# Kernel optimization log

Hardware: AMD Instinct MI355X
Metric: run time of the kernel (lower is better)

Reference implementation:

```python
import jax, jax.numpy as jnp
import numpy as np

C_IN = 1.0
C_OUT = 1.0
N_NODES = 10000
D_IN = 256
D_OUT = 256
N_EDGES = 320000
MIN_NORM = 1e-15
BALL_EPS = 4e-3  # float32 boundary eps used by HGCN PoincareBall


def _norm(x):
    return jnp.maximum(jnp.linalg.norm(x, axis=-1, keepdims=True), MIN_NORM)


def _artanh(x):
    x = jnp.clip(x, -1.0 + 1e-7, 1.0 - 1e-7)
    return 0.5 * (jnp.log1p(x) - jnp.log1p(-x))


def proj(x, c):
    norm = _norm(x)
    maxnorm = (1.0 - BALL_EPS) / jnp.sqrt(c)
    return jnp.where(norm > maxnorm, x / norm * maxnorm, x)


def expmap0(u, c):
    sc = jnp.sqrt(c)
    un = _norm(u)
    return jnp.tanh(sc * un) * u / (sc * un)


def logmap0(p, c):
    sc = jnp.sqrt(c)
    pn = _norm(p)
    return _artanh(sc * pn) * p / (sc * pn)


def mobius_add(x, y, c):
    x2 = jnp.sum(x * x, -1, keepdims=True)
    y2 = jnp.sum(y * y, -1, keepdims=True)
    xy = jnp.sum(x * y, -1, keepdims=True)
    num = (1 + 2 * c * xy + c * y2) * x + (1 - c * x2) * y
    denom = 1 + 2 * c * xy + c * c * x2 * y2
    return num / jnp.maximum(denom, MIN_NORM)


def mobius_matvec(m, x, c):
    sc = jnp.sqrt(c)
    xn = _norm(x)
    mx = x @ m.T  # [N, D_out]
    mxn = _norm(mx)
    res = jnp.tanh(mxn / xn * _artanh(sc * xn)) * mx / (mxn * sc)
    cond = jnp.all(mx == 0, axis=-1, keepdims=True)
    return jnp.where(cond, jnp.zeros_like(res), res)


def setup_inputs() -> dict:
    key = jax.random.key(0)
    k = jax.random.split(key, 6)
    x = jax.random.normal(k[0], (N_NODES, D_IN), jnp.float32) * 0.05
    x = proj(x, C_IN)  # valid points on the Poincare ball
    weight = jax.random.normal(k[1], (D_OUT, D_IN), jnp.float32) * (1.0 / np.sqrt(D_IN))
    bias = jax.random.normal(k[2], (D_OUT,), jnp.float32) * 0.01
    adj_val = jax.random.uniform(k[3], (N_EDGES,), jnp.float32) * (1.0 / 32.0)
    adj_row = jnp.sort(jax.random.randint(k[4], (N_EDGES,), 0, N_NODES, jnp.int32))
    adj_col = jax.random.randint(k[5], (N_EDGES,), 0, N_NODES, jnp.int32)
    return {"x": x, "weight": weight, "bias": bias, "adj_val": adj_val,
            "adj_row": adj_row, "adj_col": adj_col}


def reference(x, weight, bias, adj_val, adj_row, adj_col):
    # --- HypLinear: mobius matvec + hyperbolic bias ---
    h = proj(mobius_matvec(weight, x, C_IN), C_IN)
    hyp_bias = proj(expmap0(bias[None, :], C_IN), C_IN)  # proj_tan0 is identity
    h = proj(mobius_add(h, hyp_bias, C_IN), C_IN)
    # --- HypAgg: tangent-space sparse aggregation ---
    x_t = logmap0(h, C_IN)  # [N, D_out]
    msgs = adj_val[:, None] * x_t[adj_col]  # [E, D_out]
    support_t = jax.ops.segment_sum(msgs, adj_row, num_segments=N_NODES)
    h = proj(expmap0(support_t, C_IN), C_IN)
    # --- HypAct: act in tangent space, remap with c_out ---
    xt = jax.nn.relu(logmap0(h, C_IN))
    return proj(expmap0(xt, C_OUT), C_OUT)
```

## Files before the change

### kernel.cpp

```cpp
#include <hip/hip_runtime.h>
#include <math.h>

#define D 256
#define MAXNORM (1.0f - 4e-3f)
#define MIN_NORM 1e-15f

typedef _Float16 v8h __attribute__((ext_vector_type(8)));
typedef _Float16 h4  __attribute__((ext_vector_type(4)));
typedef float    v4f __attribute__((ext_vector_type(4)));

__device__ __forceinline__ float wave_reduce_sum(float v) {
    #pragma unroll
    for (int m = 32; m >= 1; m >>= 1) v += __shfl_xor(v, m, 64);
    return v;
}

__device__ __forceinline__ float dot4(const float4& a, const float4& b) {
    return a.x * b.x + a.y * b.y + a.z * b.z + a.w * b.w;
}

__device__ __forceinline__ float artanh_clip(float x) {
    x = fminf(fmaxf(x, -1.0f + 1e-7f), 1.0f - 1e-7f);
    return 0.5f * (log1pf(x) - log1pf(-x));
}

__global__ __launch_bounds__(256) void prep_kernel(
    const float* __restrict__ bias, const float* __restrict__ W,
    const int* __restrict__ rows,
    float* __restrict__ HB, _Float16* __restrict__ Wh,
    int* __restrict__ rowptr, int N, int E)
{
    const int b = blockIdx.x, t = threadIdx.x;
    const int e = b * 256 + t;

    if (e < E) {
        int r1 = rows[e];
        if (e == 0) {
            for (int r = 0; r <= r1; ++r) rowptr[r] = 0;
        } else {
            int r0 = rows[e - 1];
            for (int r = r0 + 1; r <= r1; ++r) rowptr[r] = e;
        }
        if (e == E - 1) {
            for (int r = r1 + 1; r <= N; ++r) rowptr[r] = E;
        }
    }

    if (b < 64) {
        int i = b * 256 + t;
        float4 v = ((const float4*)W)[i];
        h4 o; o[0] = (_Float16)v.x; o[1] = (_Float16)v.y;
        o[2] = (_Float16)v.z; o[3] = (_Float16)v.w;
        *(h4*)(Wh + 4 * (size_t)i) = o;
    }

    if (b == 64 && t < 64) {
        int l = t;
        float4 v = *(const float4*)(bias + 4 * l);
        float bn = fmaxf(sqrtf(wave_reduce_sum(dot4(v, v))), MIN_NORM);
        float f = tanhf(bn) / bn;
        float4 h = make_float4(v.x * f, v.y * f, v.z * f, v.w * f);
        float hn = fmaxf(sqrtf(wave_reduce_sum(dot4(h, h))), MIN_NORM);
        float s = (hn > MAXNORM) ? (MAXNORM / hn) : 1.0f;
        h.x *= s; h.y *= s; h.z *= s; h.w *= s;
        *(float4*)(HB + 4 * l) = h;
        float y2 = wave_reduce_sum(dot4(h, h));
        if (l == 0) HB[D] = y2;
    }
}

#define AS16 264

__global__ __launch_bounds__(256) void gemmrow_kernel(
    const float* __restrict__ X, const _Float16* __restrict__ Wh,
    const float* __restrict__ HB, _Float16* __restrict__ XT, int N)
{
    __shared__ _Float16 As[16 * AS16];
    __shared__ float xnsq[16];
    __shared__ float part_s[16][4];
    __shared__ float part_d[16][4];
    __shared__ float Arow[16], Brow[16];

    const int t = threadIdx.x;
    const int r0 = blockIdx.x * 16;

    {
        const int r = t >> 4, q2 = t & 15;
        const int grow = r0 + r;
        float ss = 0.0f;
        #pragma unroll
        for (int j = 0; j < 4; ++j) {
            const int fi = q2 + j * 16;
            float4 v = make_float4(0.f, 0.f, 0.f, 0.f);
            if (grow < N) v = ((const float4*)X)[(size_t)grow * 64 + fi];
            ss += dot4(v, v);
            h4 hv; hv[0] = (_Float16)v.x; hv[1] = (_Float16)v.y;
            hv[2] = (_Float16)v.z; hv[3] = (_Float16)v.w;
            *(h4*)&As[r * AS16 + fi * 4] = hv;
        }
        ss += __shfl_xor(ss, 1, 64);
        ss += __shfl_xor(ss, 2, 64);
        ss += __shfl_xor(ss, 4, 64);
        ss += __shfl_xor(ss, 8, 64);
        if (q2 == 0) xnsq[r] = ss;
    }
    __syncthreads();

    const int w  = t >> 6;
    const int l  = t & 63;
    const int lm = l & 15;
    const int q  = l >> 4;

    v4f acc[4];
    #pragma unroll
    for (int ct = 0; ct < 4; ++ct)
        #pragma unroll
        for (int i = 0; i < 4; ++i) acc[ct][i] = 0.0f;

    const _Float16* WhB = Wh + (size_t)(64 * w + lm) * 256 + q * 8;

    #pragma unroll
    for (int kc = 0; kc < 8; ++kc) {
        v8h a = *(const v8h*)&As[lm * AS16 + kc * 32 + q * 8];
        #pragma unroll
        for (int ct = 0; ct < 4; ++ct) {
            v8h bfr = *(const v8h*)(WhB + (size_t)ct * 16 * 256 + kc * 32);
            acc[ct] = __builtin_amdgcn_mfma_f32_16x16x32_f16(a, bfr, acc[ct], 0, 0, 0);
        }
    }

    float yv[4];
    #pragma unroll
    for (int ct = 0; ct < 4; ++ct) yv[ct] = HB[64 * w + ct * 16 + lm];

    {
        float s_[4], d_[4];
        #pragma unroll
        for (int i = 0; i < 4; ++i) {
            float s = 0.f, d = 0.f;
            #pragma unroll
            for (int ct = 0; ct < 4; ++ct) {
                float v = acc[ct][i];
                s = fmaf(v, v, s);
                d = fmaf(v, yv[ct], d);
            }
            #pragma unroll
            for (int m = 1; m <= 8; m <<= 1) {
                s += __shfl_xor(s, m, 64);
                d += __shfl_xor(d, m, 64);
            }
            s_[i] = s; d_[i] = d;
        }
        if (lm == 0) {
            #pragma unroll
            for (int i = 0; i < 4; ++i) {
                part_s[q * 4 + i][w] = s_[i];
                part_d[q * 4 + i][w] = d_[i];
            }
        }
    }
    __syncthreads();

    if (t < 16) {
        float mx2 = part_s[t][0] + part_s[t][1] + part_s[t][2] + part_s[t][3];
        float mxy = part_d[t][0] + part_d[t][1] + part_d[t][2] + part_d[t][3];
        float y2  = HB[D];
        float xn  = fmaxf(sqrtf(xnsq[t]), MIN_NORM);
        float mxn = fmaxf(sqrtf(mx2), MIN_NORM);
        float r  = (mxn / xn) * artanh_clip(xn);
        float th = tanhf(r);
        float f  = th / mxn;
        float hn = fmaxf(th, MIN_NORM);
        float s  = (hn > MAXNORM) ? (MAXNORM / hn) : 1.0f;
        float fs = f * s;
        float x2 = th * th * s * s;
        float xy  = fs * mxy;
        float ch  = 1.0f + 2.0f * xy + y2;
        float cy  = 1.0f - x2;
        float inv = 1.0f / fmaxf(1.0f + 2.0f * xy + x2 * y2, MIN_NORM);
        float alpha = ch * fs * inv;
        float beta  = cy * inv;
        float gss = alpha * alpha * mx2 + 2.0f * alpha * beta * mxy + beta * beta * y2;
        float gn  = fmaxf(sqrtf(gss), MIN_NORM);
        float s2  = (gn > MAXNORM) ? (MAXNORM / gn) : 1.0f;
        float pn  = fmaxf(gn * s2, MIN_NORM);
        float lf  = artanh_clip(pn) / pn;
        Arow[t] = lf * s2 * alpha;
        Brow[t] = lf * s2 * beta;
    }
    __syncthreads();

    #pragma unroll
    for (int i = 0; i < 4; ++i) {
        const int rr = q * 4 + i;
        const int row = r0 + rr;
        if (row < N) {
            float A = Arow[rr], B = Brow[rr];
            #pragma unroll
            for (int ct = 0; ct < 4; ++ct) {
                float v = fmaf(A, acc[ct][i], B * yv[ct]);
                XT[(size_t)row * 256 + 64 * w + ct * 16 + lm] = (_Float16)v;
            }
        }
    }
}

__global__ __launch_bounds__(256) void agg_kernel(
    const int* __restrict__ rowptr, const int* __restrict__ cols,
    const float* __restrict__ vals, const _Float16* __restrict__ XT,
    float* __restrict__ OUT, int N)
{
    const int wq = __builtin_amdgcn_readfirstlane(threadIdx.x >> 6);
    const int node = blockIdx.x * 4 + wq;
    const int l = threadIdx.x & 63;
    if (node >= N) return;

    const int start = rowptr[node];
    const int end   = rowptr[node + 1];

    const h4* xt4 = (const h4*)XT;
    float4 acc = make_float4(0.f, 0.f, 0.f, 0.f);

    for (int g = start; g < end; g += 16) {
        int   cbuf[16];
        float vbuf[16];
        #pragma unroll
        for (int u = 0; u < 16; ++u) {
            int ee = g + u;
            bool ok = ee < end;
            int ec = ok ? ee : (end - 1);
            cbuf[u] = cols[ec];
            vbuf[u] = ok ? vals[ec] : 0.0f;
        }
        h4 m[16];
        #pragma unroll
        for (int u = 0; u < 16; ++u)
            m[u] = xt4[(size_t)cbuf[u] * 64 + l];
        #pragma unroll
        for (int u = 0; u < 16; ++u) {
            acc.x = fmaf(vbuf[u], (float)m[u][0], acc.x);
            acc.y = fmaf(vbuf[u], (float)m[u][1], acc.y);
            acc.z = fmaf(vbuf[u], (float)m[u][2], acc.z);
            acc.w = fmaf(vbuf[u], (float)m[u][3], acc.w);
        }
    }

    float un = fmaxf(sqrtf(wave_reduce_sum(dot4(acc, acc))), MIN_NORM);
    float f = tanhf(un) / un;
    float4 h = make_float4(acc.x * f, acc.y * f, acc.z * f, acc.w * f);
    float hn = fmaxf(sqrtf(wave_reduce_sum(dot4(h, h))), MIN_NORM);
    float s = (hn > MAXNORM) ? (MAXNORM / hn) : 1.0f;
    h.x *= s; h.y *= s; h.z *= s; h.w *= s;
    float pn = fmaxf(hn * s, MIN_NORM);
    float lf = artanh_clip(pn) / pn;
    float4 tt = make_float4(fmaxf(h.x * lf, 0.f), fmaxf(h.y * lf, 0.f),
                            fmaxf(h.z * lf, 0.f), fmaxf(h.w * lf, 0.f));
    float un2 = fmaxf(sqrtf(wave_reduce_sum(dot4(tt, tt))), MIN_NORM);
    float f2 = tanhf(un2) / un2;
    float4 o = make_float4(tt.x * f2, tt.y * f2, tt.z * f2, tt.w * f2);
    float on = fmaxf(sqrtf(wave_reduce_sum(dot4(o, o))), MIN_NORM);
    float s2 = (on > MAXNORM) ? (MAXNORM / on) : 1.0f;

    v4f ov;
    ov[0] = o.x * s2; ov[1] = o.y * s2; ov[2] = o.z * s2; ov[3] = o.w * s2;
    __builtin_nontemporal_store(ov, (v4f*)(OUT + (size_t)node * D + 4 * l));
}

extern "C" void kernel_launch(void* const* d_in, const int* in_sizes, int n_in,
                              void* d_out, int out_size, void* d_ws, size_t ws_size,
                              hipStream_t stream) {
    const float* X    = (const float*)d_in[0];
    const float* W    = (const float*)d_in[1];
    const float* bias = (const float*)d_in[2];
    const float* vals = (const float*)d_in[3];
    const int*   rows = (const int*)d_in[4];
    const int*   cols = (const int*)d_in[5];
    float* OUT = (float*)d_out;

    const int N = in_sizes[0] / D;
    const int E = in_sizes[3];

    int*      rowptr = (int*)d_ws;
    float*    HB = (float*)d_ws + 10240;
    _Float16* Wh = (_Float16*)((float*)d_ws + 10240 + 512);
    _Float16* XT = (_Float16*)((float*)d_ws + 10240 + 512 + 32768);

    prep_kernel<<<(E + 255) / 256, 256, 0, stream>>>(bias, W, rows, HB, Wh, rowptr, N, E);
    gemmrow_kernel<<<(N + 15) / 16, 256, 0, stream>>>(X, Wh, HB, XT, N);
    int wave_blocks = (N + 3) / 4;
    agg_kernel<<<wave_blocks, 256, 0, stream>>>(rowptr, cols, vals, XT, OUT, N);
}
```

Baseline: 110.9 us.

## Fuse prep, GEMM and aggregation into one cooperative kernel with grid syncs

```diff
diff --git a/kernel.cpp b/kernel.cpp
--- a/kernel.cpp
+++ b/kernel.cpp
@@ -1,9 +1,13 @@
 #include <hip/hip_runtime.h>
+#include <hip/hip_cooperative_groups.h>
 #include <math.h>
+
+namespace cg = cooperative_groups;
 
 #define D 256
 #define MAXNORM (1.0f - 4e-3f)
 #define MIN_NORM 1e-15f
+#define COOP_GRID 512
 
 typedef _Float16 v8h __attribute__((ext_vector_type(8)));
 typedef _Float16 h4  __attribute__((ext_vector_type(4)));
@@ -22,6 +26,245 @@
 __device__ __forceinline__ float artanh_clip(float x) {
     x = fminf(fmaxf(x, -1.0f + 1e-7f), 1.0f - 1e-7f);
     return 0.5f * (log1pf(x) - log1pf(-x));
+}
+
+#define AS16 264
+
+__global__ __launch_bounds__(256, 2) void fused_coop_kernel(
+    const float* __restrict__ X, const float* __restrict__ W,
+    const float* __restrict__ bias, const float* __restrict__ vals,
+    const int* __restrict__ rows, const int* __restrict__ cols,
+    int* __restrict__ rowptr, _Float16* __restrict__ Wh,
+    float* __restrict__ HB, _Float16* __restrict__ XT,
+    float* __restrict__ OUT, int N, int E)
+{
+    __shared__ _Float16 As[16 * AS16];
+    __shared__ float xnsq[16];
+    __shared__ float part_s[16][4];
+    __shared__ float part_d[16][4];
+    __shared__ float Arow[16], Brow[16];
+
+    const int bid = blockIdx.x;
+    const int t = threadIdx.x;
+
+    for (int e = bid * 256 + t; e < E; e += COOP_GRID * 256) {
+        int r1 = rows[e];
+        if (e == 0) {
+            for (int r = 0; r <= r1; ++r) rowptr[r] = 0;
+        } else {
+            int rp = rows[e - 1];
+            for (int r = rp + 1; r <= r1; ++r) rowptr[r] = e;
+        }
+        if (e == E - 1) {
+            for (int r = r1 + 1; r <= N; ++r) rowptr[r] = E;
+        }
+    }
+    {
+        int i = bid * 256 + t;
+        if (i < 16384) {
+            float4 v = ((const float4*)W)[i];
+            h4 o; o[0] = (_Float16)v.x; o[1] = (_Float16)v.y;
+            o[2] = (_Float16)v.z; o[3] = (_Float16)v.w;
+            *(h4*)(Wh + 4 * (size_t)i) = o;
+        }
+    }
+    if (bid == 0 && t < 64) {
+        int l = t;
+        float4 v = *(const float4*)(bias + 4 * l);
+        float bn = fmaxf(sqrtf(wave_reduce_sum(dot4(v, v))), MIN_NORM);
+        float f = tanhf(bn) / bn;
+        float4 h = make_float4(v.x * f, v.y * f, v.z * f, v.w * f);
+        float hn = fmaxf(sqrtf(wave_reduce_sum(dot4(h, h))), MIN_NORM);
+        float s = (hn > MAXNORM) ? (MAXNORM / hn) : 1.0f;
+        h.x *= s; h.y *= s; h.z *= s; h.w *= s;
+        *(float4*)(HB + 4 * l) = h;
+        float y2 = wave_reduce_sum(dot4(h, h));
+        if (l == 0) HB[D] = y2;
+    }
+
+    cg::this_grid().sync();
+
+    const int NT = (N + 15) / 16;
+    const int w  = t >> 6;
+    const int l  = t & 63;
+    const int lm = l & 15;
+    const int q  = l >> 4;
+
+    for (int tile = bid; tile < NT; tile += COOP_GRID) {
+        const int r0 = tile * 16;
+
+        {
+            const int r = t >> 4, q2 = t & 15;
+            const int grow = r0 + r;
+            float ss = 0.0f;
+            #pragma unroll
+            for (int j = 0; j < 4; ++j) {
+                const int fi = q2 + j * 16;
+                float4 v = make_float4(0.f, 0.f, 0.f, 0.f);
+                if (grow < N) v = ((const float4*)X)[(size_t)grow * 64 + fi];
+                ss += dot4(v, v);
+                h4 hv; hv[0] = (_Float16)v.x; hv[1] = (_Float16)v.y;
+                hv[2] = (_Float16)v.z; hv[3] = (_Float16)v.w;
+                *(h4*)&As[r * AS16 + fi * 4] = hv;
+            }
+            ss += __shfl_xor(ss, 1, 64);
+            ss += __shfl_xor(ss, 2, 64);
+            ss += __shfl_xor(ss, 4, 64);
+            ss += __shfl_xor(ss, 8, 64);
+            if (q2 == 0) xnsq[r] = ss;
+        }
+        __syncthreads();
+
+        v4f acc[4];
+        #pragma unroll
+        for (int ct = 0; ct < 4; ++ct)
+            #pragma unroll
+            for (int i = 0; i < 4; ++i) acc[ct][i] = 0.0f;
+
+        const _Float16* WhB = Wh + (size_t)(64 * w + lm) * 256 + q * 8;
+
+        #pragma unroll
+        for (int kc = 0; kc < 8; ++kc) {
+            v8h a = *(const v8h*)&As[lm * AS16 + kc * 32 + q * 8];
+            #pragma unroll
+            for (int ct = 0; ct < 4; ++ct) {
+                v8h bfr = *(const v8h*)(WhB + (size_t)ct * 16 * 256 + kc * 32);
+                acc[ct] = __builtin_amdgcn_mfma_f32_16x16x32_f16(a, bfr, acc[ct], 0, 0, 0);
+            }
+        }
+
+        float yv[4];
+        #pragma unroll
+        for (int ct = 0; ct < 4; ++ct) yv[ct] = HB[64 * w + ct * 16 + lm];
+
+        {
+            float s_[4], d_[4];
+            #pragma unroll
+            for (int i = 0; i < 4; ++i) {
+                float s = 0.f, d = 0.f;
+                #pragma unroll
+                for (int ct = 0; ct < 4; ++ct) {
+                    float v = acc[ct][i];
+                    s = fmaf(v, v, s);
+                    d = fmaf(v, yv[ct], d);
+                }
+                #pragma unroll
+                for (int m = 1; m <= 8; m <<= 1) {
+                    s += __shfl_xor(s, m, 64);
+                    d += __shfl_xor(d, m, 64);
+                }
+                s_[i] = s; d_[i] = d;
+            }
+            if (lm == 0) {
+                #pragma unroll
+                for (int i = 0; i < 4; ++i) {
+                    part_s[q * 4 + i][w] = s_[i];
+                    part_d[q * 4 + i][w] = d_[i];
+                }
+            }
+        }
+        __syncthreads();
+
+        if (t < 16) {
+            float mx2 = part_s[t][0] + part_s[t][1] + part_s[t][2] + part_s[t][3];
+            float mxy = part_d[t][0] + part_d[t][1] + part_d[t][2] + part_d[t][3];
+            float y2  = HB[D];
+            float xn  = fmaxf(sqrtf(xnsq[t]), MIN_NORM);
+            float mxn = fmaxf(sqrtf(mx2), MIN_NORM);
+            float r  = (mxn / xn) * artanh_clip(xn);
+            float th = tanhf(r);
+            float f  = th / mxn;
+            float hn = fmaxf(th, MIN_NORM);
+            float s  = (hn > MAXNORM) ? (MAXNORM / hn) : 1.0f;
+            float fs = f * s;
+            float x2 = th * th * s * s;
+            float xy  = fs * mxy;
+            float ch  = 1.0f + 2.0f * xy + y2;
+            float cy  = 1.0f - x2;
+            float inv = 1.0f / fmaxf(1.0f + 2.0f * xy + x2 * y2, MIN_NORM);
+            float alpha = ch * fs * inv;
+            float beta  = cy * inv;
+            float gss = alpha * alpha * mx2 + 2.0f * alpha * beta * mxy + beta * beta * y2;
+            float gn  = fmaxf(sqrtf(gss), MIN_NORM);
+            float s2  = (gn > MAXNORM) ? (MAXNORM / gn) : 1.0f;
+            float pn  = fmaxf(gn * s2, MIN_NORM);
+            float lf  = artanh_clip(pn) / pn;
+            Arow[t] = lf * s2 * alpha;
+            Brow[t] = lf * s2 * beta;
+        }
+        __syncthreads();
+
+        #pragma unroll
+        for (int i = 0; i < 4; ++i) {
+            const int rr = q * 4 + i;
+            const int row = r0 + rr;
+            if (row < N) {
+                float A = Arow[rr], B = Brow[rr];
+                #pragma unroll
+                for (int ct = 0; ct < 4; ++ct) {
+                    float v = fmaf(A, acc[ct][i], B * yv[ct]);
+                    XT[(size_t)row * 256 + 64 * w + ct * 16 + lm] = (_Float16)v;
+                }
+            }
+        }
+        __syncthreads();
+    }
+
+    cg::this_grid().sync();
+
+    const int wq = __builtin_amdgcn_readfirstlane(t >> 6);
+    const h4* xt4 = (const h4*)XT;
+
+    for (int node = bid * 4 + wq; node < N; node += COOP_GRID * 4) {
+        const int start = rowptr[node];
+        const int end   = rowptr[node + 1];
+
+        float4 acc2 = make_float4(0.f, 0.f, 0.f, 0.f);
+
+        for (int g = start; g < end; g += 16) {
+            int   cbuf[16];
+            float vbuf[16];
+            #pragma unroll
+            for (int u = 0; u < 16; ++u) {
+                int ee = g + u;
+                bool ok = ee < end;
+                int ec = ok ? ee : (end - 1);
+                cbuf[u] = cols[ec];
+                vbuf[u] = ok ? vals[ec] : 0.0f;
+            }
+            h4 m[16];
+            #pragma unroll
+            for (int u = 0; u < 16; ++u)
+                m[u] = xt4[(size_t)cbuf[u] * 64 + l];
+            #pragma unroll
+            for (int u = 0; u < 16; ++u) {
+                acc2.x = fmaf(vbuf[u], (float)m[u][0], acc2.x);
+                acc2.y = fmaf(vbuf[u], (float)m[u][1], acc2.y);
+                acc2.z = fmaf(vbuf[u], (float)m[u][2], acc2.z);
+                acc2.w = fmaf(vbuf[u], (float)m[u][3], acc2.w);
+            }
+        }
+
+        float un = fmaxf(sqrtf(wave_reduce_sum(dot4(acc2, acc2))), MIN_NORM);
+        float f = tanhf(un) / un;
+        float4 h = make_float4(acc2.x * f, acc2.y * f, acc2.z * f, acc2.w * f);
+        float hn = fmaxf(sqrtf(wave_reduce_sum(dot4(h, h))), MIN_NORM);
+        float s = (hn > MAXNORM) ? (MAXNORM / hn) : 1.0f;
+        h.x *= s; h.y *= s; h.z *= s; h.w *= s;
+        float pn = fmaxf(hn * s, MIN_NORM);
+        float lf = artanh_clip(pn) / pn;
+        float4 tt = make_float4(fmaxf(h.x * lf, 0.f), fmaxf(h.y * lf, 0.f),
+                                fmaxf(h.z * lf, 0.f), fmaxf(h.w * lf, 0.f));
+        float un2 = fmaxf(sqrtf(wave_reduce_sum(dot4(tt, tt))), MIN_NORM);
+        float f2 = tanhf(un2) / un2;
+        float4 o = make_float4(tt.x * f2, tt.y * f2, tt.z * f2, tt.w * f2);
+        float on = fmaxf(sqrtf(wave_reduce_sum(dot4(o, o))), MIN_NORM);
+        float s2 = (on > MAXNORM) ? (MAXNORM / on) : 1.0f;
+
+        v4f ov;
+        ov[0] = o.x * s2; ov[1] = o.y * s2; ov[2] = o.z * s2; ov[3] = o.w * s2;
+        __builtin_nontemporal_store(ov, (v4f*)(OUT + (size_t)node * D + 4 * l));
+    }
 }
 
 __global__ __launch_bounds__(256) void prep_kernel(
@@ -32,20 +275,12 @@
 {
     const int b = blockIdx.x, t = threadIdx.x;
     const int e = b * 256 + t;
-
     if (e < E) {
         int r1 = rows[e];
-        if (e == 0) {
-            for (int r = 0; r <= r1; ++r) rowptr[r] = 0;
-        } else {
-            int r0 = rows[e - 1];
-            for (int r = r0 + 1; r <= r1; ++r) rowptr[r] = e;
-        }
-        if (e == E - 1) {
-            for (int r = r1 + 1; r <= N; ++r) rowptr[r] = E;
-        }
-    }
-
+        if (e == 0) { for (int r = 0; r <= r1; ++r) rowptr[r] = 0; }
+        else { int r0 = rows[e - 1]; for (int r = r0 + 1; r <= r1; ++r) rowptr[r] = e; }
+        if (e == E - 1) { for (int r = r1 + 1; r <= N; ++r) rowptr[r] = E; }
+    }
     if (b < 64) {
         int i = b * 256 + t;
         float4 v = ((const float4*)W)[i];
@@ -53,7 +288,6 @@
         o[2] = (_Float16)v.z; o[3] = (_Float16)v.w;
         *(h4*)(Wh + 4 * (size_t)i) = o;
     }
-
     if (b == 64 && t < 64) {
         int l = t;
         float4 v = *(const float4*)(bias + 4 * l);
@@ -69,8 +303,6 @@
     }
 }
 
-#define AS16 264
-
 __global__ __launch_bounds__(256) void gemmrow_kernel(
     const float* __restrict__ X, const _Float16* __restrict__ Wh,
     const float* __restrict__ HB, _Float16* __restrict__ XT, int N)
@@ -83,7 +315,6 @@
 
     const int t = threadIdx.x;
     const int r0 = blockIdx.x * 16;
-
     {
         const int r = t >> 4, q2 = t & 15;
         const int grow = r0 + r;
@@ -118,7 +349,6 @@
         for (int i = 0; i < 4; ++i) acc[ct][i] = 0.0f;
 
     const _Float16* WhB = Wh + (size_t)(64 * w + lm) * 256 + q * 8;
-
     #pragma unroll
     for (int kc = 0; kc < 8; ++kc) {
         v8h a = *(const v8h*)&As[lm * AS16 + kc * 32 + q * 8];
@@ -217,7 +447,6 @@
 
     const int start = rowptr[node];
     const int end   = rowptr[node + 1];
-
     const h4* xt4 = (const h4*)XT;
     float4 acc = make_float4(0.f, 0.f, 0.f, 0.f);
 
@@ -277,16 +506,25 @@
     const int*   cols = (const int*)d_in[5];
     float* OUT = (float*)d_out;
 
-    const int N = in_sizes[0] / D;
-    const int E = in_sizes[3];
+    int N = in_sizes[0] / D;
+    int E = in_sizes[3];
 
     int*      rowptr = (int*)d_ws;
     float*    HB = (float*)d_ws + 10240;
     _Float16* Wh = (_Float16*)((float*)d_ws + 10240 + 512);
     _Float16* XT = (_Float16*)((float*)d_ws + 10240 + 512 + 32768);
 
-    prep_kernel<<<(E + 255) / 256, 256, 0, stream>>>(bias, W, rows, HB, Wh, rowptr, N, E);
-    gemmrow_kernel<<<(N + 15) / 16, 256, 0, stream>>>(X, Wh, HB, XT, N);
-    int wave_blocks = (N + 3) / 4;
-    agg_kernel<<<wave_blocks, 256, 0, stream>>>(rowptr, cols, vals, XT, OUT, N);
-}
+    void* args[] = {(void*)&X, (void*)&W, (void*)&bias, (void*)&vals,
+                    (void*)&rows, (void*)&cols, (void*)&rowptr, (void*)&Wh,
+                    (void*)&HB, (void*)&XT, (void*)&OUT, (void*)&N, (void*)&E};
+    hipError_t err = hipLaunchCooperativeKernel(
+        (const void*)fused_coop_kernel, dim3(COOP_GRID), dim3(256),
+        args, 0, stream);
+
+    if (err != hipSuccess) {
+        prep_kernel<<<(E + 255) / 256, 256, 0, stream>>>(bias, W, rows, HB, Wh, rowptr, N, E);
+        gemmrow_kernel<<<(N + 15) / 16, 256, 0, stream>>>(X, Wh, HB, XT, N);
+        int wave_blocks = (N + 3) / 4;
+        agg_kernel<<<wave_blocks, 256, 0, stream>>>(rowptr, cols, vals, XT, OUT, N);
+    }
+}
```

New measurement: 235.3 us. 112% more time.
